# Kernel optimization log

Measured on AMD Instinct MI355X. Metric: run time of the kernel, lower is better.

Reference implementation:

```python
import jax, jax.numpy as jnp
import numpy as np

DT = 1e-4  # integration step, matches Model(dt=0.0001)
T = 4_000_000


def setup_inputs() -> dict:
    key = jax.random.key(0)
    ks = jax.random.split(key, 8)
    inputs = jax.random.normal(ks[0], (1, T, 3), dtype=jnp.float32)
    # time column made increasing (as in a real signal record)
    t = jnp.arange(T, dtype=jnp.float32) * DT
    inputs = inputs.at[0, :, 0].set(t)
    # small-scale 2x2 system matrices; A shifted toward -0.5*I so the
    # 4M-step linear recurrence is stable (no overflow over long horizons)
    A = -0.5 * jnp.eye(2, dtype=jnp.float32) + 0.05 * jax.random.normal(ks[1], (2, 2), jnp.float32)
    B = 0.1 * jax.random.normal(ks[2], (2, 2), jnp.float32)
    D = 0.1 * jax.random.normal(ks[3], (2, 2), jnp.float32)
    E = 0.1 * jax.random.normal(ks[4], (2, 2), jnp.float32)
    cov_in = 0.1 * jax.random.normal(ks[5], (2, 2), jnp.float32)
    training_params = jax.random.normal(ks[6], (1, 2), jnp.float32)
    initial_states = jnp.zeros((1, 5), dtype=jnp.float32)
    return {"inputs": inputs, "A": A, "B": B, "D": D, "E": E,
            "cov_in": cov_in, "training_params": training_params,
            "initial_states": initial_states}


def reference(inputs, A, B, D, E, cov_in, training_params, initial_states):
    # Faithful to GRCell.call: cov = cov_in every step (new_cov is discarded),
    # so XiCov / XiCovC / transition matrix are time-invariant constants.
    dt = jnp.float32(DT)
    sqrt2 = jnp.sqrt(jnp.float32(2.0))
    x_signal = jnp.array([1.0, 0.0], dtype=inputs.dtype)
    XiCov = (E - cov_in @ B) / sqrt2                      # (2,2)
    XiCovC = XiCov @ (-sqrt2 * B.T)                       # (2,2)
    Trans = jnp.eye(2, dtype=inputs.dtype) + (A - XiCovC) * dt  # I + (A-XiCovC)dt
    Cout = -sqrt2 * B.T * dt                              # output map, (2,2)
    p0 = training_params[0, 0]
    p1 = training_params[0, 1]
    seq = inputs[0]                                       # [T, 3] = (time, dy1, dy2)

    def step(x, inp):
        t = inp[0]
        dy = inp[1:]
        out = Cout @ x                                    # emitted BEFORE update
        x_new = Trans @ x + XiCov @ dy + (p0 * jnp.cos(p1 * t) * dt) * x_signal
        return x_new, out

    x0 = initial_states[0, :2]
    _, outs = jax.lax.scan(step, x0, seq)                 # outs: [T, 2]
    return outs[None]                                     # [1, T, 2]
```

## Files before the change

### kernel.cpp

```cpp
#include <hip/hip_runtime.h>
#include <math.h>


constexpr int   TN    = 4000000;
constexpr float FDT   = 1e-4f;
constexpr int   L     = 16;
constexpr int   K     = TN / L;
constexpr int   BT    = 256;
constexpr int   NT    = (K + BT - 1) / BT;
constexpr int   ROWF4 = 9;
constexpr int   F4IN  = TN * 3 / 4;
constexpr int   F4OUT = TN * 2 / 4;

struct Consts {
  float T00, T01, T10, T11;
  float X00, X01, X10, X11;
  float C00, C01, C10, C11;
  float p0, p1;
};

__device__ inline Consts make_consts(const float* __restrict__ A,
                                     const float* __restrict__ B,
                                     const float* __restrict__ E,
                                     const float* __restrict__ cov,
                                     const float* __restrict__ tp) {
  const float s2 = 1.41421356237309515f;
  Consts c;
  float Xi[2][2];
  for (int i = 0; i < 2; ++i)
    for (int j = 0; j < 2; ++j)
      Xi[i][j] = (E[i*2+j] - (cov[i*2+0]*B[0*2+j] + cov[i*2+1]*B[1*2+j])) / s2;
  float XiC[2][2];
  for (int i = 0; i < 2; ++i)
    for (int j = 0; j < 2; ++j)
      XiC[i][j] = Xi[i][0]*(-s2*B[j*2+0]) + Xi[i][1]*(-s2*B[j*2+1]);
  c.T00 = 1.0f + (A[0] - XiC[0][0]) * FDT;
  c.T01 =        (A[1] - XiC[0][1]) * FDT;
  c.T10 =        (A[2] - XiC[1][0]) * FDT;
  c.T11 = 1.0f + (A[3] - XiC[1][1]) * FDT;
  c.X00 = Xi[0][0]; c.X01 = Xi[0][1]; c.X10 = Xi[1][0]; c.X11 = Xi[1][1];
  c.C00 = -s2 * B[0] * FDT;
  c.C01 = -s2 * B[2] * FDT;
  c.C10 = -s2 * B[1] * FDT;
  c.C11 = -s2 * B[3] * FDT;
  c.p0 = tp[0]; c.p1 = tp[1];
  return c;
}

__device__ inline void step(float& x0, float& x1, float t, float a, float b,
                            const Consts& c) {
  float u0 = fmaf(c.X00, a, fmaf(c.X01, b, c.p0 * __cosf(c.p1 * t) * FDT));
  float u1 = fmaf(c.X10, a, c.X11 * b);
  float n0 = fmaf(c.T00, x0, fmaf(c.T01, x1, u0));
  float n1 = fmaf(c.T10, x0, fmaf(c.T11, x1, u1));
  x0 = n0; x1 = n1;
}

__device__ inline void fsq(float* M) {
  float a = M[0]*M[0] + M[1]*M[2];
  float b = M[0]*M[1] + M[1]*M[3];
  float d = M[2]*M[0] + M[3]*M[2];
  float e = M[2]*M[1] + M[3]*M[3];
  M[0] = a; M[1] = b; M[2] = d; M[3] = e;
}

__device__ inline void mulleft(const float* P, float* M) {
  float a0 = P[0]*M[0] + P[1]*M[2];
  float a1 = P[0]*M[1] + P[1]*M[3];
  float a2 = P[2]*M[0] + P[3]*M[2];
  float a3 = P[2]*M[1] + P[3]*M[3];
  M[0]=a0; M[1]=a1; M[2]=a2; M[3]=a3;
}

__device__ inline void powmat8(const float* M, int e, float* R) {
  float C[4] = {M[0], M[1], M[2], M[3]};
  R[0] = 1.f; R[1] = 0.f; R[2] = 0.f; R[3] = 1.f;
  #pragma unroll
  for (int b = 0; b < 8; ++b) {
    if ((e >> b) & 1) mulleft(C, R);
    fsq(C);
  }
}

__global__ void __launch_bounds__(BT, 4)
k1(const float* __restrict__ seq, const float* __restrict__ A,
   const float* __restrict__ B, const float* __restrict__ E,
   const float* __restrict__ cov, const float* __restrict__ tp,
   float2* __restrict__ agg) {
  __shared__ float wg[4][2];
  const int tid  = threadIdx.x;
  const int lane = tid & 63;
  const int w    = tid >> 6;
  const int tile = blockIdx.x;
  Consts c = make_consts(A, B, E, cov, tp);

  const float4* s4 = (const float4*)seq;
  const size_t base = (size_t)tile * 3072 + 3 * tid;
  const float4 z4 = make_float4(0.f, 0.f, 0.f, 0.f);
  float4 v[12];
  #pragma unroll
  for (int it = 0; it < 4; ++it) {
    size_t g = base + (size_t)(it * 768);
    v[3*it+0] = (g     < (size_t)F4IN) ? s4[g]     : z4;
    v[3*it+1] = (g + 1 < (size_t)F4IN) ? s4[g + 1] : z4;
    v[3*it+2] = (g + 2 < (size_t)F4IN) ? s4[g + 2] : z4;
  }

  float S[4] = {c.T00, c.T01, c.T10, c.T11};
  fsq(S); fsq(S);
  float R[4];
  powmat8(S, 255 - tid, R);
  float S256[4] = {S[0], S[1], S[2], S[3]};
  #pragma unroll
  for (int i = 0; i < 8; ++i) fsq(S256);

  float acc0 = 0.f, acc1 = 0.f;
  #pragma unroll
  for (int it = 3; it >= 0; --it) {
    float x0 = 0.f, x1 = 0.f;
    const float4 a = v[3*it], b = v[3*it+1], d = v[3*it+2];
    const int st0 = tile * 4096 + 1024 * it + 4 * tid;
    step(x0, x1, (float)(st0    ) * FDT, a.y, a.z, c);
    step(x0, x1, (float)(st0 + 1) * FDT, b.x, b.y, c);
    step(x0, x1, (float)(st0 + 2) * FDT, b.w, d.x, c);
    step(x0, x1, (float)(st0 + 3) * FDT, d.z, d.w, c);
    if (it != 3) mulleft(S256, R);
    acc0 += R[0]*x0 + R[1]*x1;
    acc1 += R[2]*x0 + R[3]*x1;
  }

  #pragma unroll
  for (int m = 1; m < 64; m <<= 1) {
    acc0 += __shfl_xor(acc0, m);
    acc1 += __shfl_xor(acc1, m);
  }
  if (lane == 0) { wg[w][0] = acc0; wg[w][1] = acc1; }
  __syncthreads();
  if (tid == 0) {
    float a0 = wg[0][0] + wg[1][0] + wg[2][0] + wg[3][0];
    float a1 = wg[0][1] + wg[1][1] + wg[2][1] + wg[3][1];
    agg[tile] = make_float2(a0, a1);
  }
}

__device__ inline void stage_tile(const float4* __restrict__ seq4, int tile,
                                  float4* __restrict__ ls, int tid) {
  const size_t base4 = (size_t)tile * 3072;
  #pragma unroll
  for (int it = 0; it < 4; ++it) {
    const int u = it * BT + tid;
    const size_t g = base4 + (size_t)(it * 768 + 3 * tid);
    float4 v0 = make_float4(0.f,0.f,0.f,0.f);
    float4 v1 = v0, v2 = v0;
    if (g     < (size_t)F4IN) v0 = seq4[g];
    if (g + 1 < (size_t)F4IN) v1 = seq4[g + 1];
    if (g + 2 < (size_t)F4IN) v2 = seq4[g + 2];
    const int st  = u >> 2;
    const int kq  = u & 3;
    const int rot = (st >> 3) & 7;
    float4* row = ls + st * ROWF4;
    row[(2*kq     + rot) & 7] = make_float4(v0.y, v0.z, v1.x, v1.y);
    row[(2*kq + 1 + rot) & 7] = make_float4(v1.w, v2.x, v2.z, v2.w);
  }
}

__global__ void __launch_bounds__(BT, 4)
k3(const float* __restrict__ seq, const float* __restrict__ A,
   const float* __restrict__ B, const float* __restrict__ E,
   const float* __restrict__ cov, const float* __restrict__ tp,
   const float* __restrict__ ini, const float2* __restrict__ agg,
   float* __restrict__ out) {
  __shared__ float4 ls[BT * ROWF4];
  __shared__ float  wg[4][2];
  __shared__ float  sY[2];
  const int tid  = threadIdx.x;
  const int lane = tid & 63;
  const int w    = tid >> 6;
  const int tile = blockIdx.x;
  Consts c = make_consts(A, B, E, cov, tp);

  stage_tile((const float4*)seq, tile, ls, tid);

  {
    float Qb[4] = {c.T00, c.T01, c.T10, c.T11};
    #pragma unroll
    for (int i = 0; i < 12; ++i) fsq(Qb);
    float i0 = 0.f, i1 = 0.f;
    float inc[4][2];
    #pragma unroll
    for (int j = 0; j < 4; ++j) {
      int idx = 4 * tid + j;
      float e0 = 0.f, e1 = 0.f;
      if (idx == 0)      { e0 = ini[0]; e1 = ini[1]; }
      else if (idx < NT) { float2 a = agg[idx-1]; e0 = a.x; e1 = a.y; }
      float n0 = fmaf(Qb[0], i0, fmaf(Qb[1], i1, e0));
      float n1 = fmaf(Qb[2], i0, fmaf(Qb[3], i1, e1));
      i0 = n0; i1 = n1;
      inc[j][0] = i0; inc[j][1] = i1;
    }
    float Q4[4] = {Qb[0], Qb[1], Qb[2], Qb[3]};
    fsq(Q4); fsq(Q4);
    float C[4] = {Q4[0], Q4[1], Q4[2], Q4[3]};
    float v0 = i0, v1 = i1;
    #pragma unroll
    for (int s = 0; s < 6; ++s) {
      int st = 1 << s;
      float p0 = __shfl_up(v0, st);
      float p1 = __shfl_up(v1, st);
      if (lane >= st) {
        float n0 = fmaf(C[0], p0, fmaf(C[1], p1, v0));
        float n1 = fmaf(C[2], p0, fmaf(C[3], p1, v1));
        v0 = n0; v1 = n1;
      }
      fsq(C);
    }
    if (lane == 63) { wg[w][0] = v0; wg[w][1] = v1; }
    __syncthreads();
    float F0 = 0.f, F1 = 0.f;
    for (int ww = 0; ww < w; ++ww) {
      float n0 = fmaf(C[0], F0, fmaf(C[1], F1, wg[ww][0]));
      float n1 = fmaf(C[2], F0, fmaf(C[3], F1, wg[ww][1]));
      F0 = n0; F1 = n1;
    }
    float q0 = __shfl_up(v0, 1);
    float q1 = __shfl_up(v1, 1);
    if (lane == 0) { q0 = 0.f; q1 = 0.f; }
    float Mq[4];
    powmat8(Q4, lane, Mq);
    float Eth0 = fmaf(Mq[0], F0, fmaf(Mq[1], F1, q0));
    float Eth1 = fmaf(Mq[2], F0, fmaf(Mq[3], F1, q1));
    if (tid == (tile >> 2)) {
      int j = tile & 3;
      float Rj[4] = {Qb[0], Qb[1], Qb[2], Qb[3]};
      for (int m = 0; m < j; ++m) mulleft(Qb, Rj);
      sY[0] = fmaf(Rj[0], Eth0, fmaf(Rj[1], Eth1, inc[j][0]));
      sY[1] = fmaf(Rj[2], Eth0, fmaf(Rj[3], Eth1, inc[j][1]));
    }
    __syncthreads();
  }

  float Pb[4] = {c.T00, c.T01, c.T10, c.T11};
  #pragma unroll
  for (int i = 0; i < 4; ++i) fsq(Pb);
  float4* row = &ls[tid * ROWF4];
  const int rot = (tid >> 3) & 7;
  const int gstep = (tile * BT + tid) * L;
  float xe0, xe1;
  {
    float x0 = 0.f, x1 = 0.f;
    #pragma unroll
    for (int q = 0; q < 8; ++q) {
      float4 d = row[(q + rot) & 7];
      step(x0, x1, (float)(gstep + 2*q)     * FDT, d.x, d.y, c);
      step(x0, x1, (float)(gstep + 2*q + 1) * FDT, d.z, d.w, c);
    }
    float C[4] = {Pb[0], Pb[1], Pb[2], Pb[3]};
    float v0 = x0, v1 = x1;
    #pragma unroll
    for (int s = 0; s < 6; ++s) {
      int st = 1 << s;
      float p0 = __shfl_up(v0, st);
      float p1 = __shfl_up(v1, st);
      if (lane >= st) {
        float n0 = fmaf(C[0], p0, fmaf(C[1], p1, v0));
        float n1 = fmaf(C[2], p0, fmaf(C[3], p1, v1));
        v0 = n0; v1 = n1;
      }
      fsq(C);
    }
    if (lane == 63) { wg[w][0] = v0; wg[w][1] = v1; }
    __syncthreads();
    float E0 = 0.f, E1 = 0.f;
    for (int ww = 0; ww < w; ++ww) {
      float n0 = fmaf(C[0], E0, fmaf(C[1], E1, wg[ww][0]));
      float n1 = fmaf(C[2], E0, fmaf(C[3], E1, wg[ww][1]));
      E0 = n0; E1 = n1;
    }
    float pv0 = __shfl_up(v0, 1);
    float pv1 = __shfl_up(v1, 1);
    if (lane == 0) { pv0 = 0.f; pv1 = 0.f; }
    float Ml[4];
    powmat8(Pb, lane, Ml);
    xe0 = fmaf(Ml[0], E0, fmaf(Ml[1], E1, pv0));
    xe1 = fmaf(Ml[2], E0, fmaf(Ml[3], E1, pv1));
  }

  float Mt[4];
  powmat8(Pb, tid, Mt);
  float y0 = sY[0], y1 = sY[1];
  float x0 = fmaf(Mt[0], y0, fmaf(Mt[1], y1, xe0));
  float x1 = fmaf(Mt[2], y0, fmaf(Mt[3], y1, xe1));

  #pragma unroll
  for (int q = 0; q < 8; ++q) {
    float4 d = row[(q + rot) & 7];
    float4 o;
    o.x = fmaf(c.C00, x0, c.C01 * x1); o.y = fmaf(c.C10, x0, c.C11 * x1);
    step(x0, x1, (float)(gstep + 2*q) * FDT, d.x, d.y, c);
    o.z = fmaf(c.C00, x0, c.C01 * x1); o.w = fmaf(c.C10, x0, c.C11 * x1);
    step(x0, x1, (float)(gstep + 2*q + 1) * FDT, d.z, d.w, c);
    row[(q + rot) & 7] = o;
  }
  __syncthreads();

  float4* out4 = (float4*)out;
  const size_t obase = (size_t)tile * 2048;
  #pragma unroll
  for (int i = 0; i < 8; ++i) {
    int lf = i * BT + tid;
    size_t g = obase + (size_t)lf;
    if (g < (size_t)F4OUT) {
      int cc = lf >> 3, s = lf & 7;
      int rc = (cc >> 3) & 7;
      out4[g] = ls[cc * ROWF4 + ((s + rc) & 7)];
    }
  }
}

extern "C" void kernel_launch(void* const* d_in, const int* in_sizes, int n_in,
                              void* d_out, int out_size, void* d_ws, size_t ws_size,
                              hipStream_t stream) {
  const float* seq = (const float*)d_in[0];
  const float* A   = (const float*)d_in[1];
  const float* B   = (const float*)d_in[2];
  const float* E   = (const float*)d_in[4];
  const float* cov = (const float*)d_in[5];
  const float* tp  = (const float*)d_in[6];
  const float* ini = (const float*)d_in[7];
  float* out = (float*)d_out;

  float2* agg = (float2*)d_ws;

  k1<<<NT, BT, 0, stream>>>(seq, A, B, E, cov, tp, agg);
  k3<<<NT, BT, 0, stream>>>(seq, A, B, E, cov, tp, ini, agg, out);
}
```

Baseline: 125.0 us.

## Fuse reduction and output passes into one cooperative kernel with grid sync

Replaces the two-kernel scheme (a per-tile aggregate pass followed by the propagate-and-emit pass) with a single cooperative kernel. Each tile is staged into LDS once, its local aggregate is computed with a wave-level scan, and a grid-wide sync publishes the tile aggregates. After the sync the same tile data is reused to emit outputs. This removes the second full read of the input and one launch boundary, at the cost of a grid barrier and the requirement that all blocks be co-resident. If the cooperative launch fails, it falls back to the old two kernels.

```diff
diff --git a/kernel.cpp b/kernel.cpp
--- a/kernel.cpp
+++ b/kernel.cpp
@@ -1,5 +1,8 @@
 #include <hip/hip_runtime.h>
+#include <hip/hip_cooperative_groups.h>
 #include <math.h>
+
+namespace cg = cooperative_groups;
 
 
 constexpr int   TN    = 4000000;
@@ -82,67 +85,6 @@
   }
 }
 
-__global__ void __launch_bounds__(BT, 4)
-k1(const float* __restrict__ seq, const float* __restrict__ A,
-   const float* __restrict__ B, const float* __restrict__ E,
-   const float* __restrict__ cov, const float* __restrict__ tp,
-   float2* __restrict__ agg) {
-  __shared__ float wg[4][2];
-  const int tid  = threadIdx.x;
-  const int lane = tid & 63;
-  const int w    = tid >> 6;
-  const int tile = blockIdx.x;
-  Consts c = make_consts(A, B, E, cov, tp);
-
-  const float4* s4 = (const float4*)seq;
-  const size_t base = (size_t)tile * 3072 + 3 * tid;
-  const float4 z4 = make_float4(0.f, 0.f, 0.f, 0.f);
-  float4 v[12];
-  #pragma unroll
-  for (int it = 0; it < 4; ++it) {
-    size_t g = base + (size_t)(it * 768);
-    v[3*it+0] = (g     < (size_t)F4IN) ? s4[g]     : z4;
-    v[3*it+1] = (g + 1 < (size_t)F4IN) ? s4[g + 1] : z4;
-    v[3*it+2] = (g + 2 < (size_t)F4IN) ? s4[g + 2] : z4;
-  }
-
-  float S[4] = {c.T00, c.T01, c.T10, c.T11};
-  fsq(S); fsq(S);
-  float R[4];
-  powmat8(S, 255 - tid, R);
-  float S256[4] = {S[0], S[1], S[2], S[3]};
-  #pragma unroll
-  for (int i = 0; i < 8; ++i) fsq(S256);
-
-  float acc0 = 0.f, acc1 = 0.f;
-  #pragma unroll
-  for (int it = 3; it >= 0; --it) {
-    float x0 = 0.f, x1 = 0.f;
-    const float4 a = v[3*it], b = v[3*it+1], d = v[3*it+2];
-    const int st0 = tile * 4096 + 1024 * it + 4 * tid;
-    step(x0, x1, (float)(st0    ) * FDT, a.y, a.z, c);
-    step(x0, x1, (float)(st0 + 1) * FDT, b.x, b.y, c);
-    step(x0, x1, (float)(st0 + 2) * FDT, b.w, d.x, c);
-    step(x0, x1, (float)(st0 + 3) * FDT, d.z, d.w, c);
-    if (it != 3) mulleft(S256, R);
-    acc0 += R[0]*x0 + R[1]*x1;
-    acc1 += R[2]*x0 + R[3]*x1;
-  }
-
-  #pragma unroll
-  for (int m = 1; m < 64; m <<= 1) {
-    acc0 += __shfl_xor(acc0, m);
-    acc1 += __shfl_xor(acc1, m);
-  }
-  if (lane == 0) { wg[w][0] = acc0; wg[w][1] = acc1; }
-  __syncthreads();
-  if (tid == 0) {
-    float a0 = wg[0][0] + wg[1][0] + wg[2][0] + wg[3][0];
-    float a1 = wg[0][1] + wg[1][1] + wg[2][1] + wg[3][1];
-    agg[tile] = make_float2(a0, a1);
-  }
-}
-
 __device__ inline void stage_tile(const float4* __restrict__ seq4, int tile,
                                   float4* __restrict__ ls, int tid) {
   const size_t base4 = (size_t)tile * 3072;
@@ -165,6 +107,235 @@
 }
 
 __global__ void __launch_bounds__(BT, 4)
+kf(const float* __restrict__ seq, const float* __restrict__ A,
+   const float* __restrict__ B, const float* __restrict__ E,
+   const float* __restrict__ cov, const float* __restrict__ tp,
+   const float* __restrict__ ini, float2* __restrict__ agg,
+   float* __restrict__ out) {
+  __shared__ float4 ls[BT * ROWF4];
+  __shared__ float  wg[4][2];
+  __shared__ float  sY[2];
+  const int tid  = threadIdx.x;
+  const int lane = tid & 63;
+  const int w    = tid >> 6;
+  const int tile = blockIdx.x;
+  Consts c = make_consts(A, B, E, cov, tp);
+
+  stage_tile((const float4*)seq, tile, ls, tid);
+  __syncthreads();
+
+  float Pb[4] = {c.T00, c.T01, c.T10, c.T11};
+  #pragma unroll
+  for (int i = 0; i < 4; ++i) fsq(Pb);
+
+  float4* row = &ls[tid * ROWF4];
+  const int rot = (tid >> 3) & 7;
+  const int gstep = (tile * BT + tid) * L;
+
+  float xe0, xe1;
+  {
+    float x0 = 0.f, x1 = 0.f;
+    #pragma unroll
+    for (int q = 0; q < 8; ++q) {
+      float4 d = row[(q + rot) & 7];
+      step(x0, x1, (float)(gstep + 2*q)     * FDT, d.x, d.y, c);
+      step(x0, x1, (float)(gstep + 2*q + 1) * FDT, d.z, d.w, c);
+    }
+    float C[4] = {Pb[0], Pb[1], Pb[2], Pb[3]};
+    float v0 = x0, v1 = x1;
+    #pragma unroll
+    for (int s = 0; s < 6; ++s) {
+      int st = 1 << s;
+      float p0 = __shfl_up(v0, st);
+      float p1 = __shfl_up(v1, st);
+      if (lane >= st) {
+        float n0 = fmaf(C[0], p0, fmaf(C[1], p1, v0));
+        float n1 = fmaf(C[2], p0, fmaf(C[3], p1, v1));
+        v0 = n0; v1 = n1;
+      }
+      fsq(C);
+    }
+    if (lane == 63) { wg[w][0] = v0; wg[w][1] = v1; }
+    __syncthreads();
+    float E0 = 0.f, E1 = 0.f;
+    for (int ww = 0; ww < w; ++ww) {
+      float n0 = fmaf(C[0], E0, fmaf(C[1], E1, wg[ww][0]));
+      float n1 = fmaf(C[2], E0, fmaf(C[3], E1, wg[ww][1]));
+      E0 = n0; E1 = n1;
+    }
+    float pv0 = __shfl_up(v0, 1);
+    float pv1 = __shfl_up(v1, 1);
+    if (lane == 0) { pv0 = 0.f; pv1 = 0.f; }
+    float Ml[4];
+    powmat8(Pb, lane, Ml);
+    xe0 = fmaf(Ml[0], E0, fmaf(Ml[1], E1, pv0));
+    xe1 = fmaf(Ml[2], E0, fmaf(Ml[3], E1, pv1));
+    if (tid == 0) {
+      float t0 = 0.f, t1 = 0.f;
+      #pragma unroll
+      for (int ww = 0; ww < 4; ++ww) {
+        float n0 = fmaf(C[0], t0, fmaf(C[1], t1, wg[ww][0]));
+        float n1 = fmaf(C[2], t0, fmaf(C[3], t1, wg[ww][1]));
+        t0 = n0; t1 = n1;
+      }
+      agg[tile] = make_float2(t0, t1);
+    }
+  }
+  __threadfence();
+  cg::this_grid().sync();
+
+  {
+    float Qb[4] = {c.T00, c.T01, c.T10, c.T11};
+    #pragma unroll
+    for (int i = 0; i < 12; ++i) fsq(Qb);
+    float i0 = 0.f, i1 = 0.f;
+    float inc[4][2];
+    #pragma unroll
+    for (int j = 0; j < 4; ++j) {
+      int idx = 4 * tid + j;
+      float e0 = 0.f, e1 = 0.f;
+      if (idx == 0)      { e0 = ini[0]; e1 = ini[1]; }
+      else if (idx < NT) { float2 a = agg[idx-1]; e0 = a.x; e1 = a.y; }
+      float n0 = fmaf(Qb[0], i0, fmaf(Qb[1], i1, e0));
+      float n1 = fmaf(Qb[2], i0, fmaf(Qb[3], i1, e1));
+      i0 = n0; i1 = n1;
+      inc[j][0] = i0; inc[j][1] = i1;
+    }
+    float Q4[4] = {Qb[0], Qb[1], Qb[2], Qb[3]};
+    fsq(Q4); fsq(Q4);
+    float C[4] = {Q4[0], Q4[1], Q4[2], Q4[3]};
+    float v0 = i0, v1 = i1;
+    #pragma unroll
+    for (int s = 0; s < 6; ++s) {
+      int st = 1 << s;
+      float p0 = __shfl_up(v0, st);
+      float p1 = __shfl_up(v1, st);
+      if (lane >= st) {
+        float n0 = fmaf(C[0], p0, fmaf(C[1], p1, v0));
+        float n1 = fmaf(C[2], p0, fmaf(C[3], p1, v1));
+        v0 = n0; v1 = n1;
+      }
+      fsq(C);
+    }
+    if (lane == 63) { wg[w][0] = v0; wg[w][1] = v1; }
+    __syncthreads();
+    float F0 = 0.f, F1 = 0.f;
+    for (int ww = 0; ww < w; ++ww) {
+      float n0 = fmaf(C[0], F0, fmaf(C[1], F1, wg[ww][0]));
+      float n1 = fmaf(C[2], F0, fmaf(C[3], F1, wg[ww][1]));
+      F0 = n0; F1 = n1;
+    }
+    float q0 = __shfl_up(v0, 1);
+    float q1 = __shfl_up(v1, 1);
+    if (lane == 0) { q0 = 0.f; q1 = 0.f; }
+    float Mq[4];
+    powmat8(Q4, lane, Mq);
+    float Eth0 = fmaf(Mq[0], F0, fmaf(Mq[1], F1, q0));
+    float Eth1 = fmaf(Mq[2], F0, fmaf(Mq[3], F1, q1));
+    if (tid == (tile >> 2)) {
+      int j = tile & 3;
+      float Rj[4] = {Qb[0], Qb[1], Qb[2], Qb[3]};
+      for (int m = 0; m < j; ++m) mulleft(Qb, Rj);
+      sY[0] = fmaf(Rj[0], Eth0, fmaf(Rj[1], Eth1, inc[j][0]));
+      sY[1] = fmaf(Rj[2], Eth0, fmaf(Rj[3], Eth1, inc[j][1]));
+    }
+    __syncthreads();
+  }
+
+  float Mt[4];
+  powmat8(Pb, tid, Mt);
+  float y0 = sY[0], y1 = sY[1];
+  float x0 = fmaf(Mt[0], y0, fmaf(Mt[1], y1, xe0));
+  float x1 = fmaf(Mt[2], y0, fmaf(Mt[3], y1, xe1));
+
+  #pragma unroll
+  for (int q = 0; q < 8; ++q) {
+    float4 d = row[(q + rot) & 7];
+    float4 o;
+    o.x = fmaf(c.C00, x0, c.C01 * x1); o.y = fmaf(c.C10, x0, c.C11 * x1);
+    step(x0, x1, (float)(gstep + 2*q) * FDT, d.x, d.y, c);
+    o.z = fmaf(c.C00, x0, c.C01 * x1); o.w = fmaf(c.C10, x0, c.C11 * x1);
+    step(x0, x1, (float)(gstep + 2*q + 1) * FDT, d.z, d.w, c);
+    row[(q + rot) & 7] = o;
+  }
+  __syncthreads();
+
+  float4* out4 = (float4*)out;
+  const size_t obase = (size_t)tile * 2048;
+  #pragma unroll
+  for (int i = 0; i < 8; ++i) {
+    int lf = i * BT + tid;
+    size_t g = obase + (size_t)lf;
+    if (g < (size_t)F4OUT) {
+      int cc = lf >> 3, s = lf & 7;
+      int rc = (cc >> 3) & 7;
+      out4[g] = ls[cc * ROWF4 + ((s + rc) & 7)];
+    }
+  }
+}
+
+__global__ void __launch_bounds__(BT, 4)
+k1(const float* __restrict__ seq, const float* __restrict__ A,
+   const float* __restrict__ B, const float* __restrict__ E,
+   const float* __restrict__ cov, const float* __restrict__ tp,
+   float2* __restrict__ agg) {
+  __shared__ float wg[4][2];
+  const int tid  = threadIdx.x;
+  const int lane = tid & 63;
+  const int w    = tid >> 6;
+  const int tile = blockIdx.x;
+  Consts c = make_consts(A, B, E, cov, tp);
+
+  const float4* s4 = (const float4*)seq;
+  const size_t base = (size_t)tile * 3072 + 3 * tid;
+  const float4 z4 = make_float4(0.f, 0.f, 0.f, 0.f);
+  float4 v[12];
+  #pragma unroll
+  for (int it = 0; it < 4; ++it) {
+    size_t g = base + (size_t)(it * 768);
+    v[3*it+0] = (g     < (size_t)F4IN) ? s4[g]     : z4;
+    v[3*it+1] = (g + 1 < (size_t)F4IN) ? s4[g + 1] : z4;
+    v[3*it+2] = (g + 2 < (size_t)F4IN) ? s4[g + 2] : z4;
+  }
+
+  float S[4] = {c.T00, c.T01, c.T10, c.T11};
+  fsq(S); fsq(S);
+  float R[4];
+  powmat8(S, 255 - tid, R);
+  float S256[4] = {S[0], S[1], S[2], S[3]};
+  #pragma unroll
+  for (int i = 0; i < 8; ++i) fsq(S256);
+
+  float acc0 = 0.f, acc1 = 0.f;
+  #pragma unroll
+  for (int it = 3; it >= 0; --it) {
+    float x0 = 0.f, x1 = 0.f;
+    const float4 a = v[3*it], b = v[3*it+1], d = v[3*it+2];
+    const int st0 = tile * 4096 + 1024 * it + 4 * tid;
+    step(x0, x1, (float)(st0    ) * FDT, a.y, a.z, c);
+    step(x0, x1, (float)(st0 + 1) * FDT, b.x, b.y, c);
+    step(x0, x1, (float)(st0 + 2) * FDT, b.w, d.x, c);
+    step(x0, x1, (float)(st0 + 3) * FDT, d.z, d.w, c);
+    if (it != 3) mulleft(S256, R);
+    acc0 += R[0]*x0 + R[1]*x1;
+    acc1 += R[2]*x0 + R[3]*x1;
+  }
+
+  #pragma unroll
+  for (int m = 1; m < 64; m <<= 1) {
+    acc0 += __shfl_xor(acc0, m);
+    acc1 += __shfl_xor(acc1, m);
+  }
+  if (lane == 0) { wg[w][0] = acc0; wg[w][1] = acc1; }
+  __syncthreads();
+  if (tid == 0) {
+    float a0 = wg[0][0] + wg[1][0] + wg[2][0] + wg[3][0];
+    float a1 = wg[0][1] + wg[1][1] + wg[2][1] + wg[3][1];
+    agg[tile] = make_float2(a0, a1);
+  }
+}
+
+__global__ void __launch_bounds__(BT, 4)
 k3(const float* __restrict__ seq, const float* __restrict__ A,
    const float* __restrict__ B, const float* __restrict__ E,
    const float* __restrict__ cov, const float* __restrict__ tp,
@@ -331,6 +502,12 @@
 
   float2* agg = (float2*)d_ws;
 
-  k1<<<NT, BT, 0, stream>>>(seq, A, B, E, cov, tp, agg);
-  k3<<<NT, BT, 0, stream>>>(seq, A, B, E, cov, tp, ini, agg, out);
-}
+  void* args[] = {(void*)&seq, (void*)&A, (void*)&B, (void*)&E, (void*)&cov,
+                  (void*)&tp,  (void*)&ini, (void*)&agg, (void*)&out};
+  hipError_t err = hipLaunchCooperativeKernel((const void*)kf, dim3(NT), dim3(BT),
+                                              args, 0, stream);
+  if (err != hipSuccess) {
+    k1<<<NT, BT, 0, stream>>>(seq, A, B, E, cov, tp, agg);
+    k3<<<NT, BT, 0, stream>>>(seq, A, B, E, cov, tp, ini, agg, out);
+  }
+}
```

Result: slower. 361.9 us (+189.6%).
